# Kernel tuning notes

Measured on AMD Instinct MI355X. Metric: run time of the kernel, lower is better.

The kernel has to match this reference:

```python
import jax, jax.numpy as jnp
import numpy as np

IN_CH = 4
OUT_CH = 64
T = 100            # max points per pillar
P_MAX = 12000      # max pillars
DX = 0.16
DY = 0.16
XMIN, YMIN, ZMIN, XMAX, YMAX, ZMAX = -40.0, -40.0, -3.0, 40.0, 40.0, 1.0
NX = int(round((XMAX - XMIN) / DX))   # 500
NY = int(round((YMAX - YMIN) / DY))   # 500
EPS = 1e-5
B, N = 2, 120000


def setup_inputs() -> dict:
    key = jax.random.key(0)
    ks = jax.random.split(key, 8)
    # realistic LiDAR-like cloud: x,y spread over the grid, z mostly in range
    xy = jax.random.normal(ks[0], (B, N, 2)) * 15.0
    z = jax.random.uniform(ks[1], (B, N, 1), minval=-3.2, maxval=1.2)
    inten = jax.random.uniform(ks[2], (B, N, 1))
    points = jnp.concatenate([xy, z, inten], axis=-1)

    def bn_params(k):
        k1, k2, k3, k4 = jax.random.split(k, 4)
        g = 1.0 + 0.1 * jax.random.normal(k1, (OUT_CH,))
        b = 0.1 * jax.random.normal(k2, (OUT_CH,))
        m = 0.1 * jax.random.normal(k3, (OUT_CH,))
        v = 0.5 + jax.random.uniform(k4, (OUT_CH,))
        return g, b, m, v

    w1 = jax.random.normal(ks[3], (OUT_CH, IN_CH + 4)) * 0.3
    w2 = jax.random.normal(ks[4], (OUT_CH, OUT_CH)) * 0.1
    g1, b1, m1, v1 = bn_params(ks[5])
    g2, b2, m2, v2 = bn_params(ks[6])
    return dict(points=points, w1=w1, g1=g1, b1=b1, m1=m1, v1=v1,
                w2=w2, g2=g2, b2=b2, m2=m2, v2=v2)


def _pillarize(pts):
    # pts: [N, 4] -> dense pillar tensor [P_MAX, T, 8], validity mask, pillar keys
    x, y, z = pts[:, 0], pts[:, 1], pts[:, 2]
    valid = (x >= XMIN) & (x < XMAX) & (y >= YMIN) & (y < YMAX) & (z >= ZMIN) & (z < ZMAX)
    xi = jnp.clip(jnp.floor((x - XMIN) / DX), 0, NX - 1).astype(jnp.int32)
    yi = jnp.clip(jnp.floor((y - YMIN) / DY), 0, NY - 1).astype(jnp.int32)
    big = jnp.int32(NX * NY)  # sentinel key for invalid points (sorts last)
    keyv = jnp.where(valid, xi * NY + yi, big)
    order = jnp.argsort(keyv)          # stable sort == torch.unique ordering
    sk = keyv[order]
    ps = pts[order]
    vs = sk < big
    n = pts.shape[0]
    idx = jnp.arange(n, dtype=jnp.int32)
    new = vs & jnp.concatenate([jnp.ones((1,), bool), sk[1:] != sk[:-1]])
    rank = jnp.cumsum(new.astype(jnp.int32)) - 1          # dense pillar id (sorted)
    p_eff = jnp.minimum(jnp.sum(new.astype(jnp.int32)), P_MAX)
    start = jax.lax.cummax(jnp.where(new, idx, jnp.int32(-1)))
    intra = idx - start                                   # slot within pillar
    keep = vs & (rank < P_MAX) & (intra < T)
    r = jnp.where(keep, rank, P_MAX)
    t = jnp.where(keep, intra, T)
    pillar_pts = jnp.zeros((P_MAX, T, IN_CH), pts.dtype).at[r, t].set(ps, mode='drop')
    keys = jnp.zeros((P_MAX,), jnp.int32).at[r].set(sk, mode='drop')
    pvalid = jnp.arange(P_MAX, dtype=jnp.int32) < p_eff
    xi_u = (keys // NY).astype(pts.dtype)
    yi_u = (keys % NY).astype(pts.dtype)
    xc = xi_u * DX + XMIN + DX / 2
    yc = yi_u * DY + YMIN + DY / 2
    # enhanced features are computed for ALL T slots (incl. empty), like the original
    x_off = pillar_pts[:, :, 0] - xc[:, None]
    y_off = pillar_pts[:, :, 1] - yc[:, None]
    xc_t = jnp.broadcast_to(xc[:, None], (P_MAX, T))
    yc_t = jnp.broadcast_to(yc[:, None], (P_MAX, T))
    enh = jnp.stack([xc_t, yc_t, x_off, y_off], axis=-1)
    pin = jnp.concatenate([pillar_pts, enh], axis=-1)     # [P_MAX, T, 8]
    return pin, pvalid, keys


def _forward(points, w1, g1, b1, m1, v1, w2, g2, b2, m2, v2):
    pin, pvalid, keys = jax.vmap(_pillarize)(points)      # [B, P_MAX, T, 8]

    def bn(h, g, b, m, v):
        return (h - m) * (g * jax.lax.rsqrt(v + EPS)) + b

    h = jax.nn.relu(bn(jnp.einsum('bptc,oc->bpto', pin, w1), g1, b1, m1, v1))
    h = jax.nn.relu(bn(jnp.einsum('bptc,oc->bpto', h, w2), g2, b2, m2, v2))
    feats = jnp.max(h, axis=2)                            # max-pool over T
    feats = jnp.where(pvalid[..., None], feats, 0.0)      # zero-pad unused pillars
    bidx = jnp.broadcast_to(jnp.arange(points.shape[0], dtype=jnp.int32)[:, None], pvalid.shape)
    xi_u = jnp.where(pvalid, keys // NY, 0)
    yi_u = jnp.where(pvalid, keys % NY, 0)
    coords = jnp.stack([bidx, xi_u, yi_u], axis=-1)       # [B, P_MAX, 3]
    return feats, coords


def reference(points, w1, g1, b1, m1, v1, w2, g2, b2, m2, v2):
    return _forward(points, w1, g1, b1, m1, v1, w2, g2, b2, m2, v2)
```

## Files before the change

### kernel.cpp

```cpp
#include <hip/hip_runtime.h>
#include <stdint.h>
#include <stddef.h>

#define NBATCH 2
#define NPTS   120000
#define T_SLOTS 100
#define PMAX   12000
#define NXG    500
#define NYG    500
#define NBINS  (NXG*NYG)
#define NCH    ((NBINS + 63)/64)
#define NG     ((NCH + 63)/64)

#define FEAT_BLOCKS 6000

#define WS_FLAGS   ((size_t)0)
#define WS_SLOT    (WS_FLAGS + (size_t)NBATCH*NBINS)
#define WS_ZEROEND (WS_SLOT  + (size_t)NBATCH*PMAX*4)
#define WS_MASKS   (WS_ZEROEND)
#define WS_PIDX    (WS_MASKS + (size_t)NBATCH*NCH*8)
#define WS_CHOFF   (WS_PIDX  + (size_t)NBATCH*PMAX*T_SLOTS*4)
#define WS_PILKEY  (WS_CHOFF + (size_t)NBATCH*NCH*4)
#define WS_GRPS    (WS_PILKEY+ (size_t)NBATCH*PMAX*4)
#define WS_PTOT    (WS_GRPS  + (size_t)NBATCH*NG*4)
#define WS_NEEDED  (WS_PTOT  + (size_t)NBATCH*4)

#define ZERO_F4    (WS_ZEROEND / 16)


__global__ void k_zero(float4* __restrict__ dst) {
    int i = blockIdx.x * blockDim.x + threadIdx.x;
    if (i < (int)ZERO_F4) {
        float4 z; z.x = 0.0f; z.y = 0.0f; z.z = 0.0f; z.w = 0.0f;
        dst[i] = z;
    }
}

__global__ void k_key(const float4* __restrict__ pts4,
                      unsigned char* __restrict__ flags) {
    int i = blockIdx.x * blockDim.x + threadIdx.x;
    if (i >= NBATCH * NPTS) return;
    int b = i / NPTS;
    float4 P = pts4[i];
    float x = P.x, y = P.y, z = P.z;
    bool valid = (x >= -40.0f) && (x < 40.0f) &&
                 (y >= -40.0f) && (y < 40.0f) &&
                 (z >= -3.0f)  && (z < 1.0f);
    if (valid) {
        float fx = floorf((x + 40.0f) / 0.16f);
        float fy = floorf((y + 40.0f) / 0.16f);
        fx = fminf(fmaxf(fx, 0.0f), (float)(NXG - 1));
        fy = fminf(fmaxf(fy, 0.0f), (float)(NYG - 1));
        int key = (int)fx * NYG + (int)fy;
        flags[(size_t)b * NBINS + key] = 1;
    }
}

__global__ __launch_bounds__(1024)
void k_scanA(const unsigned char* __restrict__ flags,
             unsigned long long* __restrict__ masks,
             int* __restrict__ grpsum) {
    __shared__ int scnt[64];
    const int g    = blockIdx.x;
    const int b    = blockIdx.y;
    const int tid  = threadIdx.x;
    const int lane = tid & 63;
    const int w    = tid >> 6;
    const unsigned char* fb = flags + (size_t)b * NBINS;

    #pragma unroll
    for (int q = 0; q < 4; ++q) {
        int chl = w * 4 + q;
        int ch  = g * 64 + chl;
        int bin = ch * 64 + lane;
        int pres = (ch < NCH && bin < NBINS && fb[bin]) ? 1 : 0;
        unsigned long long m = __ballot(pres);
        if (lane == 0) {
            if (ch < NCH) masks[(size_t)b * NCH + ch] = m;
            scnt[chl] = __popcll(m);
        }
    }
    __syncthreads();
    if (w == 0) {
        int v = scnt[lane];
        #pragma unroll
        for (int off = 32; off > 0; off >>= 1) v += __shfl_xor(v, off);
        if (lane == 0) grpsum[b * NG + g] = v;
    }
}

__global__ void k_choff(const unsigned long long* __restrict__ masks,
                        const int* __restrict__ grpsum,
                        int* __restrict__ choff, int* __restrict__ ptot) {
    int tid  = threadIdx.x;
    int lane = tid & 63;
    int gw   = blockIdx.x * 4 + (tid >> 6);
    if (gw >= NBATCH * NG) return;
    int b = gw / NG, g = gw - b * NG;

    int gs = (lane < NG) ? grpsum[b * NG + lane] : 0;
    int incl = gs;
    #pragma unroll
    for (int off = 1; off < 64; off <<= 1) {
        int t2 = __shfl_up(incl, off);
        if (lane >= off) incl += t2;
    }
    int tot  = __shfl(incl, NG - 1);
    int goff = __shfl(incl, (g == 0) ? 0 : g - 1);
    if (g == 0) goff = 0;
    if (g == 0 && lane == 0) ptot[b] = tot;

    int ch = g * 64 + lane;
    int cs = (ch < NCH) ? __popcll(masks[(size_t)b * NCH + ch]) : 0;
    int incl2 = cs;
    #pragma unroll
    for (int off = 1; off < 64; off <<= 1) {
        int t2 = __shfl_up(incl2, off);
        if (lane >= off) incl2 += t2;
    }
    if (ch < NCH) choff[(size_t)b * NCH + ch] = goff + incl2 - cs;
}

__global__ void k_fill(const float4* __restrict__ pts4,
                       const unsigned long long* __restrict__ masks,
                       const int* __restrict__ choff, int* __restrict__ slotctr,
                       int* __restrict__ pilkey, int* __restrict__ pidx) {
    int i = blockIdx.x * blockDim.x + threadIdx.x;
    if (i >= NBATCH * NPTS) return;
    int b = i / NPTS;
    int j = i - b * NPTS;
    float4 P = pts4[i];
    float x = P.x, y = P.y, z = P.z;
    bool valid = (x >= -40.0f) && (x < 40.0f) &&
                 (y >= -40.0f) && (y < 40.0f) &&
                 (z >= -3.0f)  && (z < 1.0f);
    if (!valid) return;
    float fx = floorf((x + 40.0f) / 0.16f);
    float fy = floorf((y + 40.0f) / 0.16f);
    fx = fminf(fmaxf(fx, 0.0f), (float)(NXG - 1));
    fy = fminf(fmaxf(fy, 0.0f), (float)(NYG - 1));
    int key = (int)fx * NYG + (int)fy;

    int ch = key >> 6;
    unsigned long long m = masks[(size_t)b * NCH + ch];
    int r = choff[(size_t)b * NCH + ch] +
            __popcll(m & ((1ULL << (key & 63)) - 1ULL));
    if (r >= PMAX) return;
    pilkey[b * PMAX + r] = key;
    int t = atomicAdd(&slotctr[b * PMAX + r], 1);
    if (t < T_SLOTS)
        pidx[((size_t)(b * PMAX + r)) * T_SLOTS + t] = j;
}

__global__ __launch_bounds__(256, 8)
void k_feats(const float4* __restrict__ pts4,
             const float* __restrict__ w1, const float* __restrict__ g1,
             const float* __restrict__ b1, const float* __restrict__ m1,
             const float* __restrict__ v1,
             const float* __restrict__ w2, const float* __restrict__ g2,
             const float* __restrict__ b2, const float* __restrict__ m2,
             const float* __restrict__ v2,
             const int* __restrict__ pilkey, const int* __restrict__ slotctr,
             const int* __restrict__ pidx, const int* __restrict__ ptot,
             float* __restrict__ out) {
    __shared__ float4 w2s[16 * 64];
    __shared__ __align__(16) float h1s[4][64];

    const int tid  = threadIdx.x;
    const int lane = tid & 63;
    const int widx = tid >> 6;
    const int o = lane;

    float* feats  = out;
    float* coords = out + (size_t)NBATCH * PMAX * 64;

    const int p = blockIdx.x * 4 + widx;
    const int b = p / PMAX;
    const int r = p - b * PMAX;

    const int* prow = pidx + (size_t)p * T_SLOTS;
    int key = pilkey[p];
    int c   = slotctr[p];
    int4 j4 = *(const int4*)prow;
    int pe = ptot[b]; if (pe > PMAX) pe = PMAX;

    float s1 = g1[o] * rsqrtf(v1[o] + 1e-5f);
    float b1f = b1[o] - m1[o] * s1;
    float w1r[8];
    {
        const float4* w14 = (const float4*)(w1 + o * 8);
        float4 a = w14[0], c4 = w14[1];
        w1r[0] = a.x * s1;  w1r[1] = a.y * s1;  w1r[2] = a.z * s1;  w1r[3] = a.w * s1;
        w1r[4] = c4.x * s1; w1r[5] = c4.y * s1; w1r[6] = c4.z * s1; w1r[7] = c4.w * s1;
    }

    float s2 = g2[o] * rsqrtf(v2[o] + 1e-5f);
    float b2f = b2[o] - m2[o] * s2;
    {
        const float4* w2row = (const float4*)(w2 + o * 64);
        #pragma unroll
        for (int it = 0; it < 4; ++it) {
            int kq = widx + it * 4;
            float4 t = w2row[kq];
            t.x *= s2; t.y *= s2; t.z *= s2; t.w *= s2;
            w2s[kq * 64 + o] = t;
        }
    }
    __syncthreads();

    size_t frow = (size_t)p * 64;
    size_t crow = (size_t)p * 3;

    if (r >= pe) {
        feats[frow + o] = 0.0f;
        if (o < 3) coords[crow + o] = (o == 0) ? (float)b : 0.0f;
        return;
    }

    int xi = key / NYG;
    int yi = key - xi * NYG;
    float xc = (float)xi * 0.16f - 40.0f + 0.08f;
    float yc = (float)yi * 0.16f - 40.0f + 0.08f;

    int pc = (c < T_SLOTS) ? c : T_SLOTS;
    int nIter = pc + ((c < T_SLOTS) ? 1 : 0);

    float acc = 0.0f;
    for (int s = 0; s < nIter; ++s) {
        float4 P;
        if (s < pc) {
            int j = (s == 0) ? j4.x : (s == 1) ? j4.y : (s == 2) ? j4.z
                  : (s == 3) ? j4.w : prow[s];
            P = pts4[(size_t)b * NPTS + j];
        } else {
            P.x = 0.0f; P.y = 0.0f; P.z = 0.0f; P.w = 0.0f;
        }
        float h = b1f;
        h += w1r[0] * P.x; h += w1r[1] * P.y;
        h += w1r[2] * P.z; h += w1r[3] * P.w;
        h += w1r[4] * xc;  h += w1r[5] * yc;
        h += w1r[6] * (P.x - xc); h += w1r[7] * (P.y - yc);
        h = fmaxf(h, 0.0f);

        h1s[widx][o] = h;
        asm volatile("s_waitcnt lgkmcnt(0)" ::: "memory");

        float a0 = b2f, a1 = 0.0f, a2 = 0.0f, a3 = 0.0f;
        #pragma unroll
        for (int kq = 0; kq < 16; ++kq) {
            float4 w  = w2s[kq * 64 + o];
            float4 hb = *(const float4*)&h1s[widx][kq * 4];
            a0 += w.x * hb.x; a1 += w.y * hb.y;
            a2 += w.z * hb.z; a3 += w.w * hb.w;
        }
        float h2 = fmaxf((a0 + a1) + (a2 + a3), 0.0f);
        acc = fmaxf(acc, h2);
    }

    feats[frow + o] = acc;
    if (o < 3)
        coords[crow + o] = (o == 0) ? (float)b : ((o == 1) ? (float)xi : (float)yi);
}


extern "C" void kernel_launch(void* const* d_in, const int* in_sizes, int n_in,
                              void* d_out, int out_size, void* d_ws, size_t ws_size,
                              hipStream_t stream) {
    if (ws_size < WS_NEEDED) return;

    const float4* pts4 = (const float4*)d_in[0];
    const float* w1  = (const float*)d_in[1];
    const float* g1  = (const float*)d_in[2];
    const float* b1  = (const float*)d_in[3];
    const float* m1  = (const float*)d_in[4];
    const float* v1  = (const float*)d_in[5];
    const float* w2  = (const float*)d_in[6];
    const float* g2  = (const float*)d_in[7];
    const float* b2  = (const float*)d_in[8];
    const float* m2  = (const float*)d_in[9];
    const float* v2  = (const float*)d_in[10];

    char* ws = (char*)d_ws;
    unsigned char* flags = (unsigned char*)(ws + WS_FLAGS);
    int*  slotctr = (int*)(ws + WS_SLOT);
    unsigned long long* masks = (unsigned long long*)(ws + WS_MASKS);
    int*  pidx    = (int*)(ws + WS_PIDX);
    int*  choff   = (int*)(ws + WS_CHOFF);
    int*  pilkey  = (int*)(ws + WS_PILKEY);
    int*  grpsum  = (int*)(ws + WS_GRPS);
    int*  ptot    = (int*)(ws + WS_PTOT);
    float* out    = (float*)d_out;

    dim3 blk256(256);
    int npt = NBATCH * NPTS;
    dim3 grdPts((npt + 255) / 256);

    hipLaunchKernelGGL(k_zero, dim3((ZERO_F4 + 255) / 256), blk256, 0, stream,
                       (float4*)(ws + WS_FLAGS));

    hipLaunchKernelGGL(k_key, grdPts, blk256, 0, stream, pts4, flags);

    hipLaunchKernelGGL(k_scanA, dim3(NG, NBATCH), dim3(1024), 0, stream,
                       flags, masks, grpsum);

    hipLaunchKernelGGL(k_choff, dim3((NBATCH * NG + 3) / 4), blk256, 0, stream,
                       masks, grpsum, choff, ptot);

    hipLaunchKernelGGL(k_fill, grdPts, blk256, 0, stream,
                       pts4, masks, choff, slotctr, pilkey, pidx);

    hipLaunchKernelGGL(k_feats, dim3(FEAT_BLOCKS), blk256, 0, stream,
                       pts4, w1, g1, b1, m1, v1, w2, g2, b2, m2, v2,
                       pilkey, slotctr, pidx, ptot, out);
}
```

Baseline: 51.38 us.

## Scatter point data directly into pillar slots and fold pillar-constant terms

The fill kernel now writes each point's full float4 into its pillar slot instead of its index, so the feature kernel reads points contiguously without a dependent index-then-gather load. The first-layer linear term is also algebraically refactored: the x/y offset weights are merged into the point weights, and the pillar-center contribution is precomputed once per pillar. This removes a dependent global load and several FMAs per point. In exchange the pillar workspace grows fourfold (16 bytes per slot) and the fill kernel does 16-byte scattered writes.

```diff
diff --git a/kernel.cpp b/kernel.cpp
--- a/kernel.cpp
+++ b/kernel.cpp
@@ -18,8 +18,8 @@
 #define WS_SLOT    (WS_FLAGS + (size_t)NBATCH*NBINS)
 #define WS_ZEROEND (WS_SLOT  + (size_t)NBATCH*PMAX*4)
 #define WS_MASKS   (WS_ZEROEND)
-#define WS_PIDX    (WS_MASKS + (size_t)NBATCH*NCH*8)
-#define WS_CHOFF   (WS_PIDX  + (size_t)NBATCH*PMAX*T_SLOTS*4)
+#define WS_PDAT    (WS_MASKS + (size_t)NBATCH*NCH*8)
+#define WS_CHOFF   (WS_PDAT  + (size_t)NBATCH*PMAX*T_SLOTS*16)
 #define WS_PILKEY  (WS_CHOFF + (size_t)NBATCH*NCH*4)
 #define WS_GRPS    (WS_PILKEY+ (size_t)NBATCH*PMAX*4)
 #define WS_PTOT    (WS_GRPS  + (size_t)NBATCH*NG*4)
@@ -124,11 +124,10 @@
 __global__ void k_fill(const float4* __restrict__ pts4,
                        const unsigned long long* __restrict__ masks,
                        const int* __restrict__ choff, int* __restrict__ slotctr,
-                       int* __restrict__ pilkey, int* __restrict__ pidx) {
+                       int* __restrict__ pilkey, float4* __restrict__ pdat) {
     int i = blockIdx.x * blockDim.x + threadIdx.x;
     if (i >= NBATCH * NPTS) return;
     int b = i / NPTS;
-    int j = i - b * NPTS;
     float4 P = pts4[i];
     float x = P.x, y = P.y, z = P.z;
     bool valid = (x >= -40.0f) && (x < 40.0f) &&
@@ -149,11 +148,11 @@
     pilkey[b * PMAX + r] = key;
     int t = atomicAdd(&slotctr[b * PMAX + r], 1);
     if (t < T_SLOTS)
-        pidx[((size_t)(b * PMAX + r)) * T_SLOTS + t] = j;
+        pdat[((size_t)(b * PMAX + r)) * T_SLOTS + t] = P;
 }
 
 __global__ __launch_bounds__(256, 8)
-void k_feats(const float4* __restrict__ pts4,
+void k_feats(const float4* __restrict__ pdat,
              const float* __restrict__ w1, const float* __restrict__ g1,
              const float* __restrict__ b1, const float* __restrict__ m1,
              const float* __restrict__ v1,
@@ -161,8 +160,7 @@
              const float* __restrict__ b2, const float* __restrict__ m2,
              const float* __restrict__ v2,
              const int* __restrict__ pilkey, const int* __restrict__ slotctr,
-             const int* __restrict__ pidx, const int* __restrict__ ptot,
-             float* __restrict__ out) {
+             const int* __restrict__ ptot, float* __restrict__ out) {
     __shared__ float4 w2s[16 * 64];
     __shared__ __align__(16) float h1s[4][64];
 
@@ -178,10 +176,9 @@
     const int b = p / PMAX;
     const int r = p - b * PMAX;
 
-    const int* prow = pidx + (size_t)p * T_SLOTS;
+    const float4* prow = pdat + (size_t)p * T_SLOTS;
     int key = pilkey[p];
     int c   = slotctr[p];
-    int4 j4 = *(const int4*)prow;
     int pe = ptot[b]; if (pe > PMAX) pe = PMAX;
 
     float s1 = g1[o] * rsqrtf(v1[o] + 1e-5f);
@@ -193,6 +190,8 @@
         w1r[0] = a.x * s1;  w1r[1] = a.y * s1;  w1r[2] = a.z * s1;  w1r[3] = a.w * s1;
         w1r[4] = c4.x * s1; w1r[5] = c4.y * s1; w1r[6] = c4.z * s1; w1r[7] = c4.w * s1;
     }
+    float wx = w1r[0] + w1r[6];
+    float wy = w1r[1] + w1r[7];
 
     float s2 = g2[o] * rsqrtf(v2[o] + 1e-5f);
     float b2f = b2[o] - m2[o] * s2;
@@ -222,6 +221,8 @@
     float xc = (float)xi * 0.16f - 40.0f + 0.08f;
     float yc = (float)yi * 0.16f - 40.0f + 0.08f;
 
+    float pb = b1f + (w1r[4] - w1r[6]) * xc + (w1r[5] - w1r[7]) * yc;
+
     int pc = (c < T_SLOTS) ? c : T_SLOTS;
     int nIter = pc + ((c < T_SLOTS) ? 1 : 0);
 
@@ -229,17 +230,13 @@
     for (int s = 0; s < nIter; ++s) {
         float4 P;
         if (s < pc) {
-            int j = (s == 0) ? j4.x : (s == 1) ? j4.y : (s == 2) ? j4.z
-                  : (s == 3) ? j4.w : prow[s];
-            P = pts4[(size_t)b * NPTS + j];
+            P = prow[s];
         } else {
             P.x = 0.0f; P.y = 0.0f; P.z = 0.0f; P.w = 0.0f;
         }
-        float h = b1f;
-        h += w1r[0] * P.x; h += w1r[1] * P.y;
+        float h = pb;
+        h += wx * P.x; h += wy * P.y;
         h += w1r[2] * P.z; h += w1r[3] * P.w;
-        h += w1r[4] * xc;  h += w1r[5] * yc;
-        h += w1r[6] * (P.x - xc); h += w1r[7] * (P.y - yc);
         h = fmaxf(h, 0.0f);
 
         h1s[widx][o] = h;
@@ -284,7 +281,7 @@
     unsigned char* flags = (unsigned char*)(ws + WS_FLAGS);
     int*  slotctr = (int*)(ws + WS_SLOT);
     unsigned long long* masks = (unsigned long long*)(ws + WS_MASKS);
-    int*  pidx    = (int*)(ws + WS_PIDX);
+    float4* pdat  = (float4*)(ws + WS_PDAT);
     int*  choff   = (int*)(ws + WS_CHOFF);
     int*  pilkey  = (int*)(ws + WS_PILKEY);
     int*  grpsum  = (int*)(ws + WS_GRPS);
@@ -307,9 +304,9 @@
                        masks, grpsum, choff, ptot);
 
     hipLaunchKernelGGL(k_fill, grdPts, blk256, 0, stream,
-                       pts4, masks, choff, slotctr, pilkey, pidx);
+                       pts4, masks, choff, slotctr, pilkey, pdat);
 
     hipLaunchKernelGGL(k_feats, dim3(FEAT_BLOCKS), blk256, 0, stream,
-                       pts4, w1, g1, b1, m1, v1, w2, g2, b2, m2, v2,
-                       pilkey, slotctr, pidx, ptot, out);
-}
+                       pdat, w1, g1, b1, m1, v1, w2, g2, b2, m2, v2,
+                       pilkey, slotctr, ptot, out);
+}
```

New measurement: 48.16 us. 6.3% less time.
